# Kernel optimization log

Hardware: AMD Instinct MI355X
Metric: run time of the kernel (lower is better)

Reference implementation:

```python
import jax, jax.numpy as jnp
import numpy as np
from jax import lax

B, HI, WI, D = 8, 64, 64, 128
HO, WO = HI // 2, WI // 2
N_IN, N_OUT = HI * WI, HO * WO
NUM_ITERS = 3
EPS = 1e-6


def _build_indices(Ho, Wo):
    # replicates _build_q_and_in_idx: per coarse position, 9 relative offsets
    dys = np.repeat(np.arange(-1, 2), 3)
    dxs = np.tile(np.arange(-1, 2), 3)
    oy = np.arange(Ho)[:, None, None]
    ox = np.arange(Wo)[None, :, None]
    ny = oy + dys
    nx = ox + dxs
    valid = (ny >= 0) & (ny < Ho) & (nx >= 0) & (nx < Wo)  # (Ho,Wo,9)
    coarse = np.where(valid, ny * Wo + nx, 0)
    base = (oy * Wo + ox) * 9
    g9 = np.where(valid, base + np.arange(9), 0).reshape(-1, 9)
    c9 = coarse.reshape(-1, 9)
    q_idx = np.stack([np.tile(g9, (1, 4))] * 4)
    col_idx = np.stack([np.tile(c9, (1, 4))] * 4)
    in_idx = np.stack([np.tile(np.where(valid, coarse * 4 + h, 0).reshape(-1, 9), (1, 4)) for h in range(4)])
    return q_idx.astype(np.int32), in_idx.astype(np.int32), col_idx.astype(np.int32)


Q_IDX, IN_IDX, COL_IDX = _build_indices(HO, WO)
# NATTEN kernel-3 neighborhoods: window center clamped to stay in-bounds.
NY = np.clip(np.arange(HO) - 1, 0, HO - 3)[:, None] + np.arange(3)  # (HO,3)
NX = np.clip(np.arange(WO) - 1, 0, WO - 3)[:, None] + np.arange(3)  # (WO,3)


def _ln(x, g, b, eps=1e-5):
    mu = x.mean(-1, keepdims=True)
    var = ((x - mu) ** 2).mean(-1, keepdims=True)
    return (x - mu) * lax.rsqrt(var + eps) * g + b


def _forward(x, seed_w, wq, wk, wv, w1, b1, w2, b2, ln_in_g, ln_in_b, ln_out_g, ln_out_b, rpb, tau):
    ny, nx = jnp.asarray(NY), jnp.asarray(NX)
    q_idx = jnp.asarray(Q_IDX)

    def unfold(t):  # (B,HI,WI,D) -> (B,4,HO,WO,D); head = ky*2+kx (F.unfold order)
        return t.reshape(B, HO, 2, WO, 2, D).transpose(0, 2, 4, 1, 3, 5).reshape(B, 4, HO, WO, D)

    k = unfold((_ln(x, ln_in_g, ln_in_b) @ wk.T).reshape(B, HI, WI, D))
    v = unfold((x @ wv.T).reshape(B, HI, WI, D))
    k_n = k[:, :, ny][:, :, :, :, nx]  # (B,4,HO,3,WO,3,D)
    v_n = v[:, :, ny][:, :, :, :, nx]

    x_map = x.reshape(B, HI, WI, D).transpose(0, 3, 1, 2)
    seed = lax.conv_general_dilated(x_map, seed_w, (2, 2), ((1, 1), (1, 1)),
                                    dimension_numbers=('NCHW', 'OIHW', 'NCHW'))
    x_out = _ln(seed.reshape(B, D, N_OUT).transpose(0, 2, 1), ln_out_g, ln_out_b)

    scale = jnp.exp(tau)
    attn36 = a_col_h = None
    for _ in range(NUM_ITERS):
        q = (_ln(x_out, ln_out_g, ln_out_b) @ wq.T).reshape(B, HO, WO, D)
        # na2d_qk (q broadcast over the 4 heads) + relative position bias
        logits = jnp.einsum('byxd,bhykxld->bhyxkl', q, k_n).reshape(B, 4, HO, WO, 9) + rpb.reshape(1, 4, 1, 1, 9)
        attn = jax.nn.softmax(logits * scale, axis=-1) + EPS
        flat = attn.reshape(B, 4, N_OUT * 9)
        attn36 = jnp.take_along_axis(
            flat, jnp.broadcast_to(q_idx.reshape(1, 4, -1), (B, 4, N_OUT * 36)), axis=-1
        ).reshape(B, 4, N_OUT, 36)
        a_col_h = attn36 / (attn36.sum(axis=(1, 3), keepdims=True) + EPS)
        attn9 = a_col_h[..., :9].reshape(B, 4, HO, WO, 3, 3)
        # na2d_av then sum over heads
        updates = jnp.einsum('bhyxkl,bhykxld->byxd', attn9, v_n).reshape(B, N_OUT, D)
        x_out = x_out + updates
        h1 = jax.nn.gelu(x_out @ w1.T + b1, approximate=False)
        x_out = x_out + _ln(h1 @ w2.T + b2, ln_out_g, ln_out_b)
    return x_out, attn36, a_col_h


def setup_inputs() -> dict:
    key = jax.random.key(0)
    ks = jax.random.split(key, 8)
    n = lambda k, shape, s: jax.random.normal(k, shape, jnp.float32) * s
    D2 = 2 * D
    return {
        'x': jax.random.normal(ks[0], (B, N_IN, D), jnp.float32),
        'seed_w': n(ks[1], (D, D, 3, 3), (2.0 / (9 * D)) ** 0.5),
        'wq': n(ks[2], (D, D), D ** -0.5),
        'wk': n(ks[3], (D, D), D ** -0.5),
        'wv': n(ks[4], (D, D), D ** -0.5),
        'w1': n(ks[5], (D2, D), D ** -0.5),
        'b1': jnp.zeros((D2,), jnp.float32),
        'w2': n(ks[6], (D, D2), D2 ** -0.5),
        'b2': jnp.zeros((D,), jnp.float32),
        'ln_in_g': jnp.ones((D,), jnp.float32),
        'ln_in_b': jnp.zeros((D,), jnp.float32),
        'ln_out_g': jnp.ones((D,), jnp.float32),
        'ln_out_b': jnp.zeros((D,), jnp.float32),
        'rpb': n(ks[7], (4, 9), 0.02),
        'tau': jnp.float32(np.log(D ** -0.5)),
    }


def reference(x, seed_w, wq, wk, wv, w1, b1, w2, b2, ln_in_g, ln_in_b, ln_out_g, ln_out_b, rpb, tau):
    x_out, attn36, a_col_h = _forward(x, seed_w, wq, wk, wv, w1, b1, w2, b2,
                                      ln_in_g, ln_in_b, ln_out_g, ln_out_b, rpb, tau)
    # A_col: scatter_add over dim 1 -> A_col[b, in_idx[i,j], j] += a_col_h[b,i,j]
    rows = jnp.asarray(IN_IDX).reshape(4 * N_OUT, 36)
    cols = jnp.broadcast_to(jnp.arange(36), rows.shape)
    A_col = jnp.zeros((B, N_IN, N_OUT), x.dtype).at[:, rows, cols].add(a_col_h.reshape(B, 4 * N_OUT, 36))
    # A_row: scatter_add over dim 2 -> A_row[b, i, col_idx[i,j]] += attn36[b,i,j]
    ri = jnp.broadcast_to(jnp.arange(4 * N_OUT)[:, None], (4 * N_OUT, 36))
    A_row = jnp.zeros((B, N_IN, N_OUT), x.dtype).at[:, ri, jnp.asarray(COL_IDX).reshape(4 * N_OUT, 36)].add(
        attn36.reshape(B, 4 * N_OUT, 36))
    return x_out, A_row, A_col
```

## Files before the change

kernel.cpp:

```cpp
#include <hip/hip_runtime.h>
#include <hip/hip_bf16.h>
#include <math.h>

#define BB   8
#define HI_  64
#define WI_  64
#define DD   128
#define HO_  32
#define WO_  32
#define NIN  4096
#define NOUT 1024
#define LN_EPS 1e-5f
#define ATT_EPS 1e-6f

typedef short bf16x8 __attribute__((ext_vector_type(8)));
typedef float f32x4  __attribute__((ext_vector_type(4)));

__device__ __forceinline__ ushort f2bf(float f) {
    union { float f; unsigned u; } a; a.f = f;
    unsigned u = a.u;
    return (ushort)((u + 0x7FFFu + ((u >> 16) & 1u)) >> 16);
}
__device__ __forceinline__ float bf2f(ushort u) {
    union { unsigned u; float f; } a; a.u = ((unsigned)u) << 16;
// ... 159 lines not shown
            for (int ks = 0; ks < 2; ++ks) {
                int kk = ks * 32 + lk;
                bf16x8 aF[2];
                aF[0] = *(const bf16x8*)&As[wm + lr][kk];
                aF[1] = *(const bf16x8*)&As[wm + 16 + lr][kk];
                #pragma unroll
                for (int ni = 0; ni < 4; ++ni) {
                    bf16x8 bF = *(const bf16x8*)&Bs[wn + ni * 16 + lr][kk];
                    acc[0][ni] = __builtin_amdgcn_mfma_f32_16x16x32_bf16(aF[0], bF, acc[0][ni], 0, 0, 0);
                    acc[1][ni] = __builtin_amdgcn_mfma_f32_16x16x32_bf16(aF[1], bF, acc[1][ni], 0, 0, 0);
                }
            }
            __syncthreads();
        }
        #pragma unroll
        for (int mi = 0; mi < 2; ++mi)
            #pragma unroll
            for (int ni = 0; ni < 4; ++ni) {
                int n = wn + ni * 16 + (lane & 15);
                #pragma unroll
                for (int r = 0; r < 4; ++r)
                    es[wm + mi * 16 + ((lane >> 4) << 2) + r][n] = acc[mi][ni][r];
            }
        __syncthreads();
        {
            int r = tid >> 2, q = tid & 3;
            float s = 0.f, s2 = 0.f;
            #pragma unroll
            for (int c = 0; c < 32; ++c) { float v = es[r][q * 32 + c]; s += v; s2 += v * v; }
            s += __shfl_down(s, 1, 64); s2 += __shfl_down(s2, 1, 64);
            s += __shfl_down(s, 2, 64); s2 += __shfl_down(s2, 2, 64);
            if (q == 0) {
                float mu = s * (1.f / DD);
                float var = s2 * (1.f / DD) - mu * mu;
                rstat[r][0] = mu; rstat[r][1] = rsqrtf(var + LN_EPS);
            }
        }
        __syncthreads();
        #pragma unroll
        for (int i = 0; i < 8; ++i) {
            int l = tid + i * 256;
            int r = l >> 5, c4 = (l & 31) << 2;
            float mu = rstat[r][0], rs = rstat[r][1];
            float4 o;
            o.x = (es[r][c4 + 0] - mu) * rs * logg[c4 + 0] + lobb[c4 + 0];
            o.y = (es[r][c4 + 1] - mu) * rs * logg[c4 + 1] + lobb[c4 + 1];
            o.z = (es[r][c4 + 2] - mu) * rs * logg[c4 + 2] + lobb[c4 + 2];
            o.w = (es[r][c4 + 3] - mu) * rs * logg[c4 + 3] + lobb[c4 + 3];
            *(float4*)(xout + (size_t)(row0 + r) * DD + c4) = o;
        }
    }
}

template<int LAST>
__global__ __launch_bounds__(512, 4)
void iter_kernel(float* __restrict__ xout, const ushort* __restrict__ kbuf,
                 const ushort* __restrict__ vbuf, const ushort* __restrict__ wqb,
                 const ushort* __restrict__ w1b, const ushort* __restrict__ w2b,
                 const float* __restrict__ b1, const float* __restrict__ b2,
                 const float* __restrict__ lg_, const float* __restrict__ lb_,
                 const float* __restrict__ rpb, const float* __restrict__ tau,
                 float* __restrict__ gbuf, float* __restrict__ denb,
                 float* __restrict__ out)
{
    const int bid = blockIdx.x;
    const int b = bid >> 6, cy = (bid >> 1) & 31, cx0 = (bid & 1) << 4;
    const int ry0 = min(max(cy - 1, 0), HO_ - 3);
    const int tid = threadIdx.x;
    const int wid = tid >> 6, lane = tid & 63;
    const int lr = lane & 15, lk = (lane >> 4) << 3;

    __shared__ float  xsf[17][132];
    __shared__ ushort Aq[32][136];
    __shared__ ushort qs[17][136];
    __shared__ float  rstat[17][2];
    __shared__ float  lgp[16][36];
    __shared__ float  lg0[36];
    __shared__ float  sm0[4];
    __shared__ ushort h1s[16][264];
    __shared__ float  es[16][132];

    for (int l = tid; l < 544; l += 512) {
        int r = l >> 5, c4 = (l & 31) << 2;
        int g = b * NOUT + (r < 16 ? cy * 32 + cx0 + r : 0);
        *(float4*)&xsf[r][c4] = *(const float4*)(xout + (size_t)g * DD + c4);
    }
    __syncthreads();
    if (tid < 68) {
        int r = tid >> 2, q = tid & 3;
        float s = 0.f, s2 = 0.f;
        #pragma unroll
        for (int c = 0; c < 32; ++c) { float v = xsf[r][q * 32 + c]; s += v; s2 += v * v; }
        s += __shfl_down(s, 1, 64); s2 += __shfl_down(s2, 1, 64);
        s += __shfl_down(s, 2, 64); s2 += __shfl_down(s2, 2, 64);
        if (q == 0) {
            float mu = s * (1.f / DD);
            float var = s2 * (1.f / DD) - mu * mu;
            rstat[r][0] = mu; rstat[r][1] = rsqrtf(var + LN_EPS);
        }
    }
    __syncthreads();
    for (int l = tid; l < 544; l += 512) {
        int r = l >> 5, c4 = (l & 31) << 2;
        float mu = rstat[r][0], rs = rstat[r][1];
        ushort4 o;
        o.x = f2bf((xsf[r][c4 + 0] - mu) * rs * lg_[c4 + 0] + lb_[c4 + 0]);
        o.y = f2bf((xsf[r][c4 + 1] - mu) * rs * lg_[c4 + 1] + lb_[c4 + 1]);
        o.z = f2bf((xsf[r][c4 + 2] - mu) * rs * lg_[c4 + 2] + lb_[c4 + 2]);
        o.w = f2bf((xsf[r][c4 + 3] - mu) * rs * lg_[c4 + 3] + lb_[c4 + 3]);
        *(ushort4*)&Aq[r][c4] = o;
    }
    for (int l = tid; l < 480; l += 512) {
        int r = 17 + (l >> 5), c4 = (l & 31) << 2;
        ushort4 z; z.x = 0; z.y = 0; z.z = 0; z.w = 0;
        *(ushort4*)&Aq[r][c4] = z;
    }
    __syncthreads();

    {
        const int wn = wid * 16;
        f32x4 acc[2] = {};
        #pragma unroll
        for (int ks = 0; ks < 4; ++ks) {
            int kk = ks * 32 + lk;
            bf16x8 aF0 = *(const bf16x8*)&Aq[lr][kk];
            bf16x8 aF1 = *(const bf16x8*)&Aq[16 + lr][kk];
            bf16x8 bF = *(const bf16x8*)(wqb + (size_t)(wn + lr) * DD + kk);
            acc[0] = __builtin_amdgcn_mfma_f32_16x16x32_bf16(aF0, bF, acc[0], 0, 0, 0);
            acc[1] = __builtin_amdgcn_mfma_f32_16x16x32_bf16(aF1, bF, acc[1], 0, 0, 0);
        }
        int n = wn + (lane & 15);
        #pragma unroll
        for (int mi = 0; mi < 2; ++mi)
            #pragma unroll
            for (int r = 0; r < 4; ++r) {
                int m = mi * 16 + ((lane >> 4) << 2) + r;
                if (m < 17) qs[m][n] = f2bf(acc[mi][r]);
            }
    }
    __syncthreads();

    for (int task = tid; task < 612; task += 512) {
        const ushort *kp, *qp;
        int cl = 0, h, jj;
        if (task < 576) {
            cl = task / 36; int t2 = task - cl * 36;
            h = t2 / 9; jj = t2 - h * 9;
            int ky = jj / 3, kx = jj - ky * 3;
            int c = cx0 + cl;
            int nx = min(max(c - 1, 0), WO_ - 3) + kx;
            kp = kbuf + (((size_t)(b * 4 + h) << 10) + (ry0 + ky) * 32 + nx) * DD;
            qp = &qs[cl][0];
        } else {
            int t2 = task - 576;
            h = t2 / 9; jj = t2 - h * 9;
            int ky = jj / 3, kx = jj - ky * 3;
            kp = kbuf + (((size_t)(b * 4 + h) << 10) + ky * 32 + kx) * DD;
            qp = &qs[16][0];
        }
        float s = 0.f;
        #pragma unroll 4
        for (int d = 0; d < 128; d += 8) {
            uint4 ku = *(const uint4*)(kp + d);
            uint4 qu = *(const uint4*)(qp + d);
            const ushort* kk2 = (const ushort*)&ku;
            const ushort* qq2 = (const ushort*)&qu;
            #pragma unroll
            for (int t = 0; t < 8; ++t) s += bf2f(kk2[t]) * bf2f(qq2[t]);
        }
        if (task < 576) lgp[cl][h * 9 + jj] = s;
        else            lg0[task - 576] = s;
    }
    __syncthreads();

    if (tid < 68) {
        float scale = expf(tau[0]);
        int h; const float* lptr; int cl = 0;
        if (tid < 64) { cl = tid >> 2; h = tid & 3; lptr = &lgp[cl][h * 9]; }
        else          { h = tid - 64; lptr = &lg0[h * 9]; }
        float tmpv[9], mx = -1e30f;
        #pragma unroll
        for (int jj = 0; jj < 9; ++jj) {
            float v = (lptr[jj] + rpb[h * 9 + jj]) * scale;
            tmpv[jj] = v; mx = fmaxf(mx, v);
        }
        float ss = 0.f;
        #pragma unroll
        for (int jj = 0; jj < 9; ++jj) { tmpv[jj] = expf(tmpv[jj] - mx); ss += tmpv[jj]; }
        float inv = 1.f / ss;
        if (tid < 64) {
            #pragma unroll
            for (int jj = 0; jj < 9; ++jj) lgp[cl][h * 9 + jj] = tmpv[jj] * inv + ATT_EPS;
        } else sm0[h] = tmpv[0] * inv + ATT_EPS;
    }
    __syncthreads();

    if (tid < 64) {
        int cl = tid >> 2, h = tid & 3;
        int c = cx0 + cl;
        float s = 0.f, gv[9];
        #pragma unroll
        for (int jj = 0; jj < 9; ++jj) {
            int dy = jj / 3 - 1, dx = jj % 3 - 1;
            bool valid = ((unsigned)(cy + dy) < (unsigned)HO_) && ((unsigned)(c + dx) < (unsigned)WO_);
            float v = valid ? lgp[cl][h * 9 + jj] : sm0[h];
            gv[jj] = v; s += v;
        }
        float tot = s;
        tot += __shfl_xor(tot, 1, 4);
        tot += __shfl_xor(tot, 2, 4);
        float dd = 4.f * tot + ATT_EPS;
        if (h == 0) denb[b * NOUT + cy * 32 + cx0 + cl] = dd;
        float inv = 1.f / dd;
        float* gp = gbuf + (((size_t)(b * 4 + h) << 10) + cy * 32 + c) * 9;
        #pragma unroll
        for (int jj = 0; jj < 9; ++jj) {
            gp[jj] = gv[jj];
            lgp[cl][h * 9 + jj] = gv[jj] * inv;
        }
    }
    __syncthreads();

    {
        int cl = tid >> 5, d0 = (tid & 31) << 2;
        int c = cx0 + cl;
        int rx0 = min(max(c - 1, 0), WO_ - 3);
        float acc4[4] = {};
        #pragma unroll
        for (int h = 0; h < 4; ++h)
            #pragma unroll
            for (int jj = 0; jj < 9; ++jj) {
                float cf = lgp[cl][h * 9 + jj];
                int ky = jj / 3, kx = jj - ky * 3;
                const ushort* vp = vbuf + (((size_t)(b * 4 + h) << 10) + (ry0 + ky) * 32 + rx0 + kx) * DD + d0;
                uint2 v0 = *(const uint2*)(vp);
                const ushort* vs0 = (const ushort*)&v0;
                #pragma unroll
                for (int t = 0; t < 4; ++t) acc4[t] += cf * bf2f(vs0[t]);
            }
        float4 o = *(float4*)&xsf[cl][d0];
        o.x += acc4[0]; o.y += acc4[1]; o.z += acc4[2]; o.w += acc4[3];
        *(float4*)&xsf[cl][d0] = o;
    }
    __syncthreads();

    {
        int l = tid;
        int r = l >> 5, c4 = (l & 31) << 2;
        ushort4 o;
        o.x = f2bf(xsf[r][c4 + 0]); o.y = f2bf(xsf[r][c4 + 1]);
        o.z = f2bf(xsf[r][c4 + 2]); o.w = f2bf(xsf[r][c4 + 3]);
        *(ushort4*)&Aq[r][c4] = o;
    }
    __syncthreads();
    {
        const int wn = wid * 32;
        f32x4 acc[2] = {};
        #pragma unroll
        for (int ks = 0; ks < 4; ++ks) {
            int kk = ks * 32 + lk;
            bf16x8 a0 = *(const bf16x8*)&Aq[lr][kk];
            #pragma unroll
            for (int ni = 0; ni < 2; ++ni) {
                bf16x8 bF = *(const bf16x8*)(w1b + (size_t)(wn + ni * 16 + lr) * DD + kk);
                acc[ni] = __builtin_amdgcn_mfma_f32_16x16x32_bf16(a0, bF, acc[ni], 0, 0, 0);
            }
        }
        #pragma unroll
        for (int ni = 0; ni < 2; ++ni) {
            int n = wn + ni * 16 + (lane & 15);
            float bv = b1[n];
            #pragma unroll
            for (int r = 0; r < 4; ++r) {
                int m = ((lane >> 4) << 2) + r;
                float v = acc[ni][r] + bv;
                v = 0.5f * v * (1.f + erff(v * 0.70710678118654752f));
                h1s[m][n] = f2bf(v);
            }
        }
    }
    __syncthreads();

    {
        const int wn = wid * 16;
        f32x4 acc = {};
        #pragma unroll
        for (int ks = 0; ks < 8; ++ks) {
            int kk = ks * 32 + lk;
            bf16x8 a0 = *(const bf16x8*)&h1s[lr][kk];
            bf16x8 bF = *(const bf16x8*)(w2b + (size_t)(wn + lr) * 256 + kk);
            acc = __builtin_amdgcn_mfma_f32_16x16x32_bf16(a0, bF, acc, 0, 0, 0);
        }
        int n = wn + (lane & 15);
        float bv = b2[n];
        #pragma unroll
        for (int r = 0; r < 4; ++r)
            es[((lane >> 4) << 2) + r][n] = acc[r] + bv;
    }
    __syncthreads();
    if (tid < 128) {
        int r = tid >> 3, qq = tid & 7;
        float s = 0.f, s2 = 0.f;
        #pragma unroll
        for (int c = 0; c < 16; ++c) { float v = es[r][qq * 16 + c]; s += v; s2 += v * v; }
        s += __shfl_down(s, 1, 64); s2 += __shfl_down(s2, 1, 64);
        s += __shfl_down(s, 2, 64); s2 += __shfl_down(s2, 2, 64);
        s += __shfl_down(s, 4, 64); s2 += __shfl_down(s2, 4, 64);
        if (qq == 0) {
            float mu = s * (1.f / DD);
            float var = s2 * (1.f / DD) - mu * mu;
            rstat[r][0] = mu; rstat[r][1] = rsqrtf(var + LN_EPS);
        }
    }
    __syncthreads();
    {
        int l = tid;
        int r = l >> 5, c4 = (l & 31) << 2;
        float mu = rstat[r][0], rs = rstat[r][1];
        size_t off = ((size_t)(b * NOUT + cy * 32 + cx0 + r)) * DD + c4;
        float4 o;
        o.x = xsf[r][c4 + 0] + (es[r][c4 + 0] - mu) * rs * lg_[c4 + 0] + lb_[c4 + 0];
        o.y = xsf[r][c4 + 1] + (es[r][c4 + 1] - mu) * rs * lg_[c4 + 1] + lb_[c4 + 1];
        o.z = xsf[r][c4 + 2] + (es[r][c4 + 2] - mu) * rs * lg_[c4 + 2] + lb_[c4 + 2];
        o.w = xsf[r][c4 + 3] + (es[r][c4 + 3] - mu) * rs * lg_[c4 + 3] + lb_[c4 + 3];
        *(float4*)(xout + off) = o;
        if (LAST) *(float4*)(out + off) = o;
    }
}

__global__ __launch_bounds__(256)
void arowcol_kernel(const float* __restrict__ gbuf, const float* __restrict__ denb,
                    float* __restrict__ Arow, float* __restrict__ Acol)
{
    const int tid = threadIdx.x;
    __shared__ int   cols[9];
    __shared__ float vals[9];
    __shared__ float wred[9][4];
    if (blockIdx.x < 32768) {
        const int bi = blockIdx.x;
        const int b = bi >> 12, i = bi & 4095;
        const int h = i >> 10, p = i & 1023;
        const int cy = p >> 5, cx = p & 31;
        if (tid < 9) {
            int dy = tid / 3 - 1, dx = tid % 3 - 1;
            bool valid = ((unsigned)(cy + dy) < (unsigned)HO_) && ((unsigned)(cx + dx) < (unsigned)WO_);
            cols[tid] = valid ? (cy + dy) * WO_ + (cx + dx) : 0;
            vals[tid] = 4.f * gbuf[(((size_t)(b * 4 + h) << 10) + p) * 9 + tid];
        }
        __syncthreads();
        float* row = Arow + (size_t)bi * NOUT;
        #pragma unroll
        for (int cc = 0; cc < 4; ++cc) {
            int c = cc * 256 + tid;
            float acc = 0.f;
            #pragma unroll
            for (int jj = 0; jj < 9; ++jj)
                if (cols[jj] == c) acc += vals[jj];
            row[c] = acc;
        }
    } else {
        const int br = blockIdx.x - 32768;
        const int b = br >> 12, r = br & 4095;
        const int h = r & 3, coarse = r >> 2;
        const int cy = coarse >> 5, cx = coarse & 31;
        if (tid < 9) {
            int dy = tid / 3 - 1, dx = tid % 3 - 1;
            int py = cy - dy, px = cx - dx;
            float v = 0.f;
            if ((unsigned)py < (unsigned)HO_ && (unsigned)px < (unsigned)WO_) {
                int p = py * WO_ + px;
                v = gbuf[(((size_t)(b * 4 + h) << 10) + p) * 9 + tid] / denb[b * NOUT + p];
            }
            vals[tid] = v;
        }
        if (r == 0) {
            float part[9] = {};
            for (int p = tid; p < NOUT; p += 256) {
                float invd = 1.f / denb[b * NOUT + p];
                int py = p >> 5, px = p & 31;
                #pragma unroll
                for (int jj = 0; jj < 9; ++jj) {
                    int dy = jj / 3 - 1, dx = jj % 3 - 1;
                    bool valid = ((unsigned)(py + dy) < (unsigned)HO_) && ((unsigned)(px + dx) < (unsigned)WO_);
                    if (!valid) part[jj] += invd;
                }
            }
            #pragma unroll
            for (int jj = 0; jj < 9; ++jj) {
                float s = part[jj];
                #pragma unroll
                for (int o = 32; o > 0; o >>= 1) s += __shfl_down(s, o, 64);
                if ((tid & 63) == 0) wred[jj][tid >> 6] = s;
            }
            __syncthreads();
            if (tid < 9) {
                float s = wred[tid][0] + wred[tid][1] + wred[tid][2] + wred[tid][3];
                float H = 0.f;
                for (int h2 = 0; h2 < 4; ++h2)
                    H += gbuf[(((size_t)(b * 4 + h2)) << 10) * 9];
                vals[tid] += H * s;
            }
        }
        __syncthreads();
        float* row = Acol + (size_t)br * NOUT;
        #pragma unroll
        for (int cc = 0; cc < 4; ++cc) {
            int c = cc * 256 + tid;
            row[c] = (c < 36) ? vals[c % 9] : 0.f;
        }
    }
}

extern "C" void kernel_launch(void* const* d_in, const int* in_sizes, int n_in,
                              void* d_out, int out_size, void* d_ws, size_t ws_size,
                              hipStream_t stream)
{
    const float* x        = (const float*)d_in[0];
    const float* seed_w   = (const float*)d_in[1];
    const float* wq       = (const float*)d_in[2];
    const float* wk       = (const float*)d_in[3];
    const float* wv       = (const float*)d_in[4];
    const float* w1       = (const float*)d_in[5];
    const float* b1       = (const float*)d_in[6];
    const float* w2       = (const float*)d_in[7];
    const float* b2       = (const float*)d_in[8];
    const float* ln_in_g  = (const float*)d_in[9];
    const float* ln_in_b  = (const float*)d_in[10];
    const float* ln_out_g = (const float*)d_in[11];
    const float* ln_out_b = (const float*)d_in[12];
    const float* rpb      = (const float*)d_in[13];
    const float* tau      = (const float*)d_in[14];

    float* out  = (float*)d_out;
    float* Arow = out + (size_t)BB * NOUT * DD;
    float* Acol = Arow + (size_t)BB * NIN * NOUT;

    float* ws    = (float*)d_ws;
    float* xout  = ws;
    float* gbuf  = xout + (size_t)BB * NOUT * DD;
    float* denb  = gbuf + (size_t)BB * 4 * NOUT * 9;
    ushort* wb   = (ushort*)(denb + BB * NOUT);
    ushort* wkb  = wb;
    ushort* wvb  = wb + 16384;
    ushort* wqb  = wb + 32768;
    ushort* w1b  = wb + 49152;
    ushort* w2b  = wb + 81920;
    ushort* wcb  = wb + 114688;

    ushort* kbuf = (ushort*)Arow;
    ushort* vbuf = kbuf + (size_t)4194304;

    wconvert_kernel<<<1024, 256, 0, stream>>>(wq, wk, wv, w1, w2, seed_w, wb);
    prep_kernel<<<640, 256, 0, stream>>>(x, wkb, wvb, wcb, ln_in_g, ln_in_b,
                                         ln_out_g, ln_out_b, kbuf, vbuf, xout);

    for (int it = 0; it < 3; ++it) {
        if (it < 2)
            iter_kernel<0><<<BB * HO_ * 2, 512, 0, stream>>>(
                xout, kbuf, vbuf, wqb, w1b, w2b, b1, b2, ln_out_g, ln_out_b,
                rpb, tau, gbuf, denb, out);
        else
            iter_kernel<1><<<BB * HO_ * 2, 512, 0, stream>>>(
                xout, kbuf, vbuf, wqb, w1b, w2b, b1, b2, ln_out_g, ln_out_b,
                rpb, tau, gbuf, denb, out);
    }

    arowcol_kernel<<<2 * BB * NIN, 256, 0, stream>>>(gbuf, denb, Arow, Acol);
}
```

Baseline: 193.6 us.

## Fuse three iteration launches into one persistent kernel with redundant query-0 row

Folds the three slot-attention iteration launches into a single kernel that keeps each block's 16 query rows in shared memory across iterations. Because every block now recomputes the coarse position 0 query (row 16) locally instead of reading it from a global buffer updated by the previous launch, the cross-block dependency disappears and the full pipeline (LN, MLP, attention) is extended to 17 rows. Block size drops from 512 to 256 threads, and the Arow/Acol writer switches to float4 stores. This removes two launches and the global round-trips of xout, at the cost of extra redundant work for the shared row and fewer threads per block.

Result: slower. 230.8 us (+19.2%).

```diff
diff --git a/kernel.cpp b/kernel.cpp
--- a/kernel.cpp
+++ b/kernel.cpp
@@ -235,16 +235,15 @@
     }
 }
 
-template<int LAST>
-__global__ __launch_bounds__(512, 4)
-void iter_kernel(float* __restrict__ xout, const ushort* __restrict__ kbuf,
-                 const ushort* __restrict__ vbuf, const ushort* __restrict__ wqb,
-                 const ushort* __restrict__ w1b, const ushort* __restrict__ w2b,
-                 const float* __restrict__ b1, const float* __restrict__ b2,
-                 const float* __restrict__ lg_, const float* __restrict__ lb_,
-                 const float* __restrict__ rpb, const float* __restrict__ tau,
-                 float* __restrict__ gbuf, float* __restrict__ denb,
-                 float* __restrict__ out)
+__global__ __launch_bounds__(256)
+void iter_all_kernel(const float* __restrict__ xout, const ushort* __restrict__ kbuf,
+                     const ushort* __restrict__ vbuf, const ushort* __restrict__ wqb,
+                     const ushort* __restrict__ w1b, const ushort* __restrict__ w2b,
+                     const float* __restrict__ b1, const float* __restrict__ b2,
+                     const float* __restrict__ lg_, const float* __restrict__ lb_,
+                     const float* __restrict__ rpb, const float* __restrict__ tau,
+                     float* __restrict__ gbuf, float* __restrict__ denb,
+                     float* __restrict__ out)
 {
     const int bid = blockIdx.x;
     const int b = bid >> 6, cy = (bid >> 1) & 31, cx0 = (bid & 1) << 4;
@@ -257,257 +256,289 @@
     __shared__ ushort Aq[32][136];
     __shared__ ushort qs[17][136];
     __shared__ float  rstat[17][2];
-    __shared__ float  lgp[16][36];
+    __shared__ float  lgp[17][36];
     __shared__ float  lg0[36];
     __shared__ float  sm0[4];
-    __shared__ ushort h1s[16][264];
-    __shared__ float  es[16][132];
-
-    for (int l = tid; l < 544; l += 512) {
+    __shared__ ushort h1s[17][264];
+    __shared__ float  es[17][132];
+
+    for (int l = tid; l < 544; l += 256) {
         int r = l >> 5, c4 = (l & 31) << 2;
         int g = b * NOUT + (r < 16 ? cy * 32 + cx0 + r : 0);
         *(float4*)&xsf[r][c4] = *(const float4*)(xout + (size_t)g * DD + c4);
     }
-    __syncthreads();
-    if (tid < 68) {
-        int r = tid >> 2, q = tid & 3;
-        float s = 0.f, s2 = 0.f;
-        #pragma unroll
-        for (int c = 0; c < 32; ++c) { float v = xsf[r][q * 32 + c]; s += v; s2 += v * v; }
-        s += __shfl_down(s, 1, 64); s2 += __shfl_down(s2, 1, 64);
-        s += __shfl_down(s, 2, 64); s2 += __shfl_down(s2, 2, 64);
-        if (q == 0) {
-            float mu = s * (1.f / DD);
-            float var = s2 * (1.f / DD) - mu * mu;
-            rstat[r][0] = mu; rstat[r][1] = rsqrtf(var + LN_EPS);
-        }
-    }
-    __syncthreads();
-    for (int l = tid; l < 544; l += 512) {
-        int r = l >> 5, c4 = (l & 31) << 2;
-        float mu = rstat[r][0], rs = rstat[r][1];
-        ushort4 o;
-        o.x = f2bf((xsf[r][c4 + 0] - mu) * rs * lg_[c4 + 0] + lb_[c4 + 0]);
-        o.y = f2bf((xsf[r][c4 + 1] - mu) * rs * lg_[c4 + 1] + lb_[c4 + 1]);
-        o.z = f2bf((xsf[r][c4 + 2] - mu) * rs * lg_[c4 + 2] + lb_[c4 + 2]);
-        o.w = f2bf((xsf[r][c4 + 3] - mu) * rs * lg_[c4 + 3] + lb_[c4 + 3]);
-        *(ushort4*)&Aq[r][c4] = o;
-    }
-    for (int l = tid; l < 480; l += 512) {
-        int r = 17 + (l >> 5), c4 = (l & 31) << 2;
-        ushort4 z; z.x = 0; z.y = 0; z.z = 0; z.w = 0;
-        *(ushort4*)&Aq[r][c4] = z;
-    }
-    __syncthreads();
-
-    {
-        const int wn = wid * 16;
-        f32x4 acc[2] = {};
-        #pragma unroll
-        for (int ks = 0; ks < 4; ++ks) {
-            int kk = ks * 32 + lk;
-            bf16x8 aF0 = *(const bf16x8*)&Aq[lr][kk];
-            bf16x8 aF1 = *(const bf16x8*)&Aq[16 + lr][kk];
-            bf16x8 bF = *(const bf16x8*)(wqb + (size_t)(wn + lr) * DD + kk);
-            acc[0] = __builtin_amdgcn_mfma_f32_16x16x32_bf16(aF0, bF, acc[0], 0, 0, 0);
-            acc[1] = __builtin_amdgcn_mfma_f32_16x16x32_bf16(aF1, bF, acc[1], 0, 0, 0);
-        }
-        int n = wn + (lane & 15);
-        #pragma unroll
-        for (int mi = 0; mi < 2; ++mi)
-            #pragma unroll
-            for (int r = 0; r < 4; ++r) {
-                int m = mi * 16 + ((lane >> 4) << 2) + r;
-                if (m < 17) qs[m][n] = f2bf(acc[mi][r]);
-            }
-    }
-    __syncthreads();
-
-    for (int task = tid; task < 612; task += 512) {
-        const ushort *kp, *qp;
-        int cl = 0, h, jj;
-        if (task < 576) {
-            cl = task / 36; int t2 = task - cl * 36;
-            h = t2 / 9; jj = t2 - h * 9;
-            int ky = jj / 3, kx = jj - ky * 3;
-            int c = cx0 + cl;
-            int nx = min(max(c - 1, 0), WO_ - 3) + kx;
-            kp = kbuf + (((size_t)(b * 4 + h) << 10) + (ry0 + ky) * 32 + nx) * DD;
-            qp = &qs[cl][0];
-        } else {
-            int t2 = task - 576;
-            h = t2 / 9; jj = t2 - h * 9;
-            int ky = jj / 3, kx = jj - ky * 3;
-            kp = kbuf + (((size_t)(b * 4 + h) << 10) + ky * 32 + kx) * DD;
-            qp = &qs[16][0];
-        }
-        float s = 0.f;
-        #pragma unroll 4
-        for (int d = 0; d < 128; d += 8) {
-            uint4 ku = *(const uint4*)(kp + d);
-            uint4 qu = *(const uint4*)(qp + d);
-            const ushort* kk2 = (const ushort*)&ku;
-            const ushort* qq2 = (const ushort*)&qu;
-            #pragma unroll
-            for (int t = 0; t < 8; ++t) s += bf2f(kk2[t]) * bf2f(qq2[t]);
-        }
-        if (task < 576) lgp[cl][h * 9 + jj] = s;
-        else            lg0[task - 576] = s;
-    }
-    __syncthreads();
-
-    if (tid < 68) {
-        float scale = expf(tau[0]);
-        int h; const float* lptr; int cl = 0;
-        if (tid < 64) { cl = tid >> 2; h = tid & 3; lptr = &lgp[cl][h * 9]; }
-        else          { h = tid - 64; lptr = &lg0[h * 9]; }
-        float tmpv[9], mx = -1e30f;
-        #pragma unroll
-        for (int jj = 0; jj < 9; ++jj) {
-            float v = (lptr[jj] + rpb[h * 9 + jj]) * scale;
-            tmpv[jj] = v; mx = fmaxf(mx, v);
-        }
-        float ss = 0.f;
-        #pragma unroll
-        for (int jj = 0; jj < 9; ++jj) { tmpv[jj] = expf(tmpv[jj] - mx); ss += tmpv[jj]; }
-        float inv = 1.f / ss;
-        if (tid < 64) {
-            #pragma unroll
-            for (int jj = 0; jj < 9; ++jj) lgp[cl][h * 9 + jj] = tmpv[jj] * inv + ATT_EPS;
-        } else sm0[h] = tmpv[0] * inv + ATT_EPS;
-    }
-    __syncthreads();
-
-    if (tid < 64) {
-        int cl = tid >> 2, h = tid & 3;
-        int c = cx0 + cl;
-        float s = 0.f, gv[9];
-        #pragma unroll
-        for (int jj = 0; jj < 9; ++jj) {
-            int dy = jj / 3 - 1, dx = jj % 3 - 1;
-            bool valid = ((unsigned)(cy + dy) < (unsigned)HO_) && ((unsigned)(c + dx) < (unsigned)WO_);
-            float v = valid ? lgp[cl][h * 9 + jj] : sm0[h];
-            gv[jj] = v; s += v;
-        }
-        float tot = s;
-        tot += __shfl_xor(tot, 1, 4);
-        tot += __shfl_xor(tot, 2, 4);
-        float dd = 4.f * tot + ATT_EPS;
-        if (h == 0) denb[b * NOUT + cy * 32 + cx0 + cl] = dd;
-        float inv = 1.f / dd;
-        float* gp = gbuf + (((size_t)(b * 4 + h) << 10) + cy * 32 + c) * 9;
-        #pragma unroll
-        for (int jj = 0; jj < 9; ++jj) {
-            gp[jj] = gv[jj];
-            lgp[cl][h * 9 + jj] = gv[jj] * inv;
-        }
-    }
-    __syncthreads();
-
-    {
-        int cl = tid >> 5, d0 = (tid & 31) << 2;
-        int c = cx0 + cl;
-        int rx0 = min(max(c - 1, 0), WO_ - 3);
-        float acc4[4] = {};
-        #pragma unroll
-        for (int h = 0; h < 4; ++h)
+
+    for (int it = 0; it < 3; ++it) {
+        __syncthreads();
+        if (tid < 68) {
+            int r = tid >> 2, q = tid & 3;
+            float s = 0.f, s2 = 0.f;
+            #pragma unroll
+            for (int c = 0; c < 32; ++c) { float v = xsf[r][q * 32 + c]; s += v; s2 += v * v; }
+            s += __shfl_down(s, 1, 64); s2 += __shfl_down(s2, 1, 64);
+            s += __shfl_down(s, 2, 64); s2 += __shfl_down(s2, 2, 64);
+            if (q == 0) {
+                float mu = s * (1.f / DD);
+                float var = s2 * (1.f / DD) - mu * mu;
+                rstat[r][0] = mu; rstat[r][1] = rsqrtf(var + LN_EPS);
+            }
+        }
+        __syncthreads();
+        for (int l = tid; l < 544; l += 256) {
+            int r = l >> 5, c4 = (l & 31) << 2;
+            float mu = rstat[r][0], rs = rstat[r][1];
+            ushort4 o;
+            o.x = f2bf((xsf[r][c4 + 0] - mu) * rs * lg_[c4 + 0] + lb_[c4 + 0]);
+            o.y = f2bf((xsf[r][c4 + 1] - mu) * rs * lg_[c4 + 1] + lb_[c4 + 1]);
+            o.z = f2bf((xsf[r][c4 + 2] - mu) * rs * lg_[c4 + 2] + lb_[c4 + 2]);
+            o.w = f2bf((xsf[r][c4 + 3] - mu) * rs * lg_[c4 + 3] + lb_[c4 + 3]);
+            *(ushort4*)&Aq[r][c4] = o;
+        }
+        __syncthreads();
+
+        {
+            const int wn = wid * 32;
+            f32x4 acc[2][2] = {};
+            #pragma unroll
+            for (int ks = 0; ks < 4; ++ks) {
+                int kk = ks * 32 + lk;
+                bf16x8 aF0 = *(const bf16x8*)&Aq[lr][kk];
+                bf16x8 aF1 = *(const bf16x8*)&Aq[16 + lr][kk];
+                #pragma unroll
+                for (int ni = 0; ni < 2; ++ni) {
+                    bf16x8 bF = *(const bf16x8*)(wqb + (size_t)(wn + ni * 16 + lr) * DD + kk);
+                    acc[0][ni] = __builtin_amdgcn_mfma_f32_16x16x32_bf16(aF0, bF, acc[0][ni], 0, 0, 0);
+                    acc[1][ni] = __builtin_amdgcn_mfma_f32_16x16x32_bf16(aF1, bF, acc[1][ni], 0, 0, 0);
+                }
+            }
+            #pragma unroll
+            for (int mi = 0; mi < 2; ++mi)
+                #pragma unroll
+                for (int ni = 0; ni < 2; ++ni) {
+                    int n = wn + ni * 16 + (lane & 15);
+                    #pragma unroll
+                    for (int r = 0; r < 4; ++r) {
+                        int m = mi * 16 + ((lane >> 4) << 2) + r;
+                        if (m < 17) qs[m][n] = f2bf(acc[mi][ni][r]);
+                    }
+                }
+        }
+        __syncthreads();
+
+        for (int task = tid; task < 612; task += 256) {
+            const ushort *kp, *qp;
+            int cl = 0, h, jj;
+            if (task < 576) {
+                cl = task / 36; int t2 = task - cl * 36;
+                h = t2 / 9; jj = t2 - h * 9;
+                int ky = jj / 3, kx = jj - ky * 3;
+                int c = cx0 + cl;
+                int nx = min(max(c - 1, 0), WO_ - 3) + kx;
+                kp = kbuf + (((size_t)(b * 4 + h) << 10) + (ry0 + ky) * 32 + nx) * DD;
+                qp = &qs[cl][0];
+            } else {
+                int t2 = task - 576;
+                h = t2 / 9; jj = t2 - h * 9;
+                int ky = jj / 3, kx = jj - ky * 3;
+                kp = kbuf + (((size_t)(b * 4 + h) << 10) + ky * 32 + kx) * DD;
+                qp = &qs[16][0];
+            }
+            float s = 0.f;
+            #pragma unroll 4
+            for (int d = 0; d < 128; d += 8) {
+                uint4 ku = *(const uint4*)(kp + d);
+                uint4 qu = *(const uint4*)(qp + d);
+                const ushort* kk2 = (const ushort*)&ku;
+                const ushort* qq2 = (const ushort*)&qu;
+                #pragma unroll
+                for (int t = 0; t < 8; ++t) s += bf2f(kk2[t]) * bf2f(qq2[t]);
+            }
+            if (task < 576) lgp[cl][h * 9 + jj] = s;
+            else            lg0[task - 576] = s;
+        }
+        __syncthreads();
+
+        if (tid < 68) {
+            float scale = expf(tau[0]);
+            int h; const float* lptr; int cl = 0;
+            if (tid < 64) { cl = tid >> 2; h = tid & 3; lptr = &lgp[cl][h * 9]; }
+            else          { h = tid - 64; lptr = &lg0[h * 9]; }
+            float tmpv[9], mx = -1e30f;
             #pragma unroll
             for (int jj = 0; jj < 9; ++jj) {
-                float cf = lgp[cl][h * 9 + jj];
-                int ky = jj / 3, kx = jj - ky * 3;
-                const ushort* vp = vbuf + (((size_t)(b * 4 + h) << 10) + (ry0 + ky) * 32 + rx0 + kx) * DD + d0;
-                uint2 v0 = *(const uint2*)(vp);
-                const ushort* vs0 = (const ushort*)&v0;
-                #pragma unroll
-                for (int t = 0; t < 4; ++t) acc4[t] += cf * bf2f(vs0[t]);
-            }
-        float4 o = *(float4*)&xsf[cl][d0];
-        o.x += acc4[0]; o.y += acc4[1]; o.z += acc4[2]; o.w += acc4[3];
-        *(float4*)&xsf[cl][d0] = o;
-    }
-    __syncthreads();
-
-    {
-        int l = tid;
-        int r = l >> 5, c4 = (l & 31) << 2;
-        ushort4 o;
-        o.x = f2bf(xsf[r][c4 + 0]); o.y = f2bf(xsf[r][c4 + 1]);
-        o.z = f2bf(xsf[r][c4 + 2]); o.w = f2bf(xsf[r][c4 + 3]);
-        *(ushort4*)&Aq[r][c4] = o;
-    }
-    __syncthreads();
-    {
-        const int wn = wid * 32;
-        f32x4 acc[2] = {};
-        #pragma unroll
-        for (int ks = 0; ks < 4; ++ks) {
-            int kk = ks * 32 + lk;
-            bf16x8 a0 = *(const bf16x8*)&Aq[lr][kk];
-            #pragma unroll
-            for (int ni = 0; ni < 2; ++ni) {
-                bf16x8 bF = *(const bf16x8*)(w1b + (size_t)(wn + ni * 16 + lr) * DD + kk);
-                acc[ni] = __builtin_amdgcn_mfma_f32_16x16x32_bf16(a0, bF, acc[ni], 0, 0, 0);
-            }
-        }
-        #pragma unroll
-        for (int ni = 0; ni < 2; ++ni) {
-            int n = wn + ni * 16 + (lane & 15);
-            float bv = b1[n];
-            #pragma unroll
-            for (int r = 0; r < 4; ++r) {
-                int m = ((lane >> 4) << 2) + r;
-                float v = acc[ni][r] + bv;
-                v = 0.5f * v * (1.f + erff(v * 0.70710678118654752f));
-                h1s[m][n] = f2bf(v);
-            }
-        }
-    }
-    __syncthreads();
-
-    {
-        const int wn = wid * 16;
-        f32x4 acc = {};
-        #pragma unroll
-        for (int ks = 0; ks < 8; ++ks) {
-            int kk = ks * 32 + lk;
-            bf16x8 a0 = *(const bf16x8*)&h1s[lr][kk];
-            bf16x8 bF = *(const bf16x8*)(w2b + (size_t)(wn + lr) * 256 + kk);
-            acc = __builtin_amdgcn_mfma_f32_16x16x32_bf16(a0, bF, acc, 0, 0, 0);
-        }
-        int n = wn + (lane & 15);
-        float bv = b2[n];
-        #pragma unroll
-        for (int r = 0; r < 4; ++r)
-            es[((lane >> 4) << 2) + r][n] = acc[r] + bv;
-    }
-    __syncthreads();
-    if (tid < 128) {
-        int r = tid >> 3, qq = tid & 7;
-        float s = 0.f, s2 = 0.f;
-        #pragma unroll
-        for (int c = 0; c < 16; ++c) { float v = es[r][qq * 16 + c]; s += v; s2 += v * v; }
-        s += __shfl_down(s, 1, 64); s2 += __shfl_down(s2, 1, 64);
-        s += __shfl_down(s, 2, 64); s2 += __shfl_down(s2, 2, 64);
-        s += __shfl_down(s, 4, 64); s2 += __shfl_down(s2, 4, 64);
-        if (qq == 0) {
-            float mu = s * (1.f / DD);
-            float var = s2 * (1.f / DD) - mu * mu;
-            rstat[r][0] = mu; rstat[r][1] = rsqrtf(var + LN_EPS);
-        }
-    }
-    __syncthreads();
-    {
-        int l = tid;
-        int r = l >> 5, c4 = (l & 31) << 2;
-        float mu = rstat[r][0], rs = rstat[r][1];
-        size_t off = ((size_t)(b * NOUT + cy * 32 + cx0 + r)) * DD + c4;
-        float4 o;
-        o.x = xsf[r][c4 + 0] + (es[r][c4 + 0] - mu) * rs * lg_[c4 + 0] + lb_[c4 + 0];
-        o.y = xsf[r][c4 + 1] + (es[r][c4 + 1] - mu) * rs * lg_[c4 + 1] + lb_[c4 + 1];
-        o.z = xsf[r][c4 + 2] + (es[r][c4 + 2] - mu) * rs * lg_[c4 + 2] + lb_[c4 + 2];
-        o.w = xsf[r][c4 + 3] + (es[r][c4 + 3] - mu) * rs * lg_[c4 + 3] + lb_[c4 + 3];
-        *(float4*)(xout + off) = o;
-        if (LAST) *(float4*)(out + off) = o;
+                float v = (lptr[jj] + rpb[h * 9 + jj]) * scale;
+                tmpv[jj] = v; mx = fmaxf(mx, v);
+            }
+            float ss = 0.f;
+            #pragma unroll
+            for (int jj = 0; jj < 9; ++jj) { tmpv[jj] = expf(tmpv[jj] - mx); ss += tmpv[jj]; }
+            float inv = 1.f / ss;
+            if (tid < 64) {
+                #pragma unroll
+                for (int jj = 0; jj < 9; ++jj) lgp[cl][h * 9 + jj] = tmpv[jj] * inv + ATT_EPS;
+            } else {
+                #pragma unroll
+                for (int jj = 0; jj < 9; ++jj) lgp[16][h * 9 + jj] = tmpv[jj] * inv + ATT_EPS;
+                sm0[h] = tmpv[0] * inv + ATT_EPS;
+            }
+        }
+        __syncthreads();
+
+        if (tid < 68) {
+            int cl = tid >> 2, h = tid & 3;
+            int ecy = (cl < 16) ? cy : 0;
+            int ec  = (cl < 16) ? (cx0 + cl) : 0;
+            float s = 0.f, gv[9];
+            #pragma unroll
+            for (int jj = 0; jj < 9; ++jj) {
+                int dy = jj / 3 - 1, dx = jj % 3 - 1;
+                bool valid = ((unsigned)(ecy + dy) < (unsigned)HO_) && ((unsigned)(ec + dx) < (unsigned)WO_);
+                float v = valid ? lgp[cl][h * 9 + jj] : sm0[h];
+                gv[jj] = v; s += v;
+            }
+            float tot = s;
+            tot += __shfl_xor(tot, 1, 4);
+            tot += __shfl_xor(tot, 2, 4);
+            float dd = 4.f * tot + ATT_EPS;
+            float inv = 1.f / dd;
+            if (it == 2 && cl < 16) {
+                if (h == 0) denb[b * NOUT + cy * 32 + cx0 + cl] = dd;
+                float* gp = gbuf + (((size_t)(b * 4 + h) << 10) + cy * 32 + ec) * 9;
+                #pragma unroll
+                for (int jj = 0; jj < 9; ++jj) gp[jj] = gv[jj];
+            }
+            #pragma unroll
+            for (int jj = 0; jj < 9; ++jj) lgp[cl][h * 9 + jj] = gv[jj] * inv;
+        }
+        __syncthreads();
+
+        for (int t = tid; t < 272; t += 256) {
+            int cl = t >> 4, d0 = (t & 15) << 3;
+            int ery0 = (cl < 16) ? ry0 : 0;
+            int erx0 = (cl < 16) ? min(max(cx0 + cl - 1, 0), WO_ - 3) : 0;
+            float acc8[8] = {};
+            #pragma unroll
+            for (int h = 0; h < 4; ++h)
+                #pragma unroll
+                for (int jj = 0; jj < 9; ++jj) {
+                    float cf = lgp[cl][h * 9 + jj];
+                    int ky = jj / 3, kx = jj - ky * 3;
+                    const ushort* vp = vbuf + (((size_t)(b * 4 + h) << 10) + (ery0 + ky) * 32 + erx0 + kx) * DD + d0;
+                    uint4 v0 = *(const uint4*)(vp);
+                    const ushort* vs0 = (const ushort*)&v0;
+                    #pragma unroll
+                    for (int e = 0; e < 8; ++e) acc8[e] += cf * bf2f(vs0[e]);
+                }
+            #pragma unroll
+            for (int e = 0; e < 8; e += 4) {
+                float4 o = *(float4*)&xsf[cl][d0 + e];
+                o.x += acc8[e]; o.y += acc8[e + 1]; o.z += acc8[e + 2]; o.w += acc8[e + 3];
+                *(float4*)&xsf[cl][d0 + e] = o;
+            }
+        }
+        __syncthreads();
+
+        for (int l = tid; l < 544; l += 256) {
+            int r = l >> 5, c4 = (l & 31) << 2;
+            ushort4 o;
+            o.x = f2bf(xsf[r][c4 + 0]); o.y = f2bf(xsf[r][c4 + 1]);
+            o.z = f2bf(xsf[r][c4 + 2]); o.w = f2bf(xsf[r][c4 + 3]);
+            *(ushort4*)&Aq[r][c4] = o;
+        }
+        __syncthreads();
+
+        {
+            const int wn = wid * 64;
+            f32x4 acc[2][4] = {};
+            #pragma unroll
+            for (int ks = 0; ks < 4; ++ks) {
+                int kk = ks * 32 + lk;
+                bf16x8 a0 = *(const bf16x8*)&Aq[lr][kk];
+                bf16x8 a1 = *(const bf16x8*)&Aq[16 + lr][kk];
+                #pragma unroll
+                for (int ni = 0; ni < 4; ++ni) {
+                    bf16x8 bF = *(const bf16x8*)(w1b + (size_t)(wn + ni * 16 + lr) * DD + kk);
+                    acc[0][ni] = __builtin_amdgcn_mfma_f32_16x16x32_bf16(a0, bF, acc[0][ni], 0, 0, 0);
+                    acc[1][ni] = __builtin_amdgcn_mfma_f32_16x16x32_bf16(a1, bF, acc[1][ni], 0, 0, 0);
+                }
+            }
+            #pragma unroll
+            for (int mi = 0; mi < 2; ++mi)
+                #pragma unroll
+                for (int ni = 0; ni < 4; ++ni) {
+                    int n = wn + ni * 16 + (lane & 15);
+                    float bv = b1[n];
+                    #pragma unroll
+                    for (int r = 0; r < 4; ++r) {
+                        int m = mi * 16 + ((lane >> 4) << 2) + r;
+                        if (m < 17) {
+                            float v = acc[mi][ni][r] + bv;
+                            v = 0.5f * v * (1.f + erff(v * 0.70710678118654752f));
+                            h1s[m][n] = f2bf(v);
+                        }
+                    }
+                }
+        }
+        __syncthreads();
+
+        {
+            const int wn = wid * 32;
+            f32x4 acc[2][2] = {};
+            #pragma unroll
+            for (int ks = 0; ks < 8; ++ks) {
+                int kk = ks * 32 + lk;
+                bf16x8 a0 = *(const bf16x8*)&h1s[lr][kk];
+                bf16x8 a1 = *(const bf16x8*)&h1s[16 + lr][kk];
+                #pragma unroll
+                for (int ni = 0; ni < 2; ++ni) {
+                    bf16x8 bF = *(const bf16x8*)(w2b + (size_t)(wn + ni * 16 + lr) * 256 + kk);
+                    acc[0][ni] = __builtin_amdgcn_mfma_f32_16x16x32_bf16(a0, bF, acc[0][ni], 0, 0, 0);
+                    acc[1][ni] = __builtin_amdgcn_mfma_f32_16x16x32_bf16(a1, bF, acc[1][ni], 0, 0, 0);
+                }
+            }
+            #pragma unroll
+            for (int mi = 0; mi < 2; ++mi)
+                #pragma unroll
+                for (int ni = 0; ni < 2; ++ni) {
+                    int n = wn + ni * 16 + (lane & 15);
+                    float bv = b2[n];
+                    #pragma unroll
+                    for (int r = 0; r < 4; ++r) {
+                        int m = mi * 16 + ((lane >> 4) << 2) + r;
+                        if (m < 17) es[m][n] = acc[mi][ni][r] + bv;
+                    }
+                }
+        }
+        __syncthreads();
+
+        if (tid < 136) {
+            int r = tid >> 3, qq = tid & 7;
+            float s = 0.f, s2 = 0.f;
+            #pragma unroll
+            for (int c = 0; c < 16; ++c) { float v = es[r][qq * 16 + c]; s += v; s2 += v * v; }
+            s += __shfl_down(s, 1, 64); s2 += __shfl_down(s2, 1, 64);
+            s += __shfl_down(s, 2, 64); s2 += __shfl_down(s2, 2, 64);
+            s += __shfl_down(s, 4, 64); s2 += __shfl_down(s2, 4, 64);
+            if (qq == 0) {
+                float mu = s * (1.f / DD);
+                float var = s2 * (1.f / DD) - mu * mu;
+                rstat[r][0] = mu; rstat[r][1] = rsqrtf(var + LN_EPS);
+            }
+        }
+        __syncthreads();
+
+        for (int l = tid; l < 544; l += 256) {
+            int r = l >> 5, c4 = (l & 31) << 2;
+            float mu = rstat[r][0], rs = rstat[r][1];
+            float4 o;
+            o.x = xsf[r][c4 + 0] + (es[r][c4 + 0] - mu) * rs * lg_[c4 + 0] + lb_[c4 + 0];
+            o.y = xsf[r][c4 + 1] + (es[r][c4 + 1] - mu) * rs * lg_[c4 + 1] + lb_[c4 + 1];
+            o.z = xsf[r][c4 + 2] + (es[r][c4 + 2] - mu) * rs * lg_[c4 + 2] + lb_[c4 + 2];
+            o.w = xsf[r][c4 + 3] + (es[r][c4 + 3] - mu) * rs * lg_[c4 + 3] + lb_[c4 + 3];
+            *(float4*)&xsf[r][c4] = o;
+            if (it == 2 && r < 16)
+                *(float4*)(out + ((size_t)(b * NOUT + cy * 32 + cx0 + r)) * DD + c4) = o;
+        }
     }
 }
 
@@ -532,15 +563,14 @@
         }
         __syncthreads();
         float* row = Arow + (size_t)bi * NOUT;
-        #pragma unroll
-        for (int cc = 0; cc < 4; ++cc) {
-            int c = cc * 256 + tid;
-            float acc = 0.f;
+        int c4 = tid << 2;
+        float o[4] = {};
+        #pragma unroll
+        for (int e = 0; e < 4; ++e)
             #pragma unroll
             for (int jj = 0; jj < 9; ++jj)
-                if (cols[jj] == c) acc += vals[jj];
-            row[c] = acc;
-        }
+                if (cols[jj] == c4 + e) o[e] += vals[jj];
+        *(float4*)(row + c4) = make_float4(o[0], o[1], o[2], o[3]);
     } else {
         const int br = blockIdx.x - 32768;
         const int b = br >> 12, r = br & 4095;
@@ -586,11 +616,14 @@
         }
         __syncthreads();
         float* row = Acol + (size_t)br * NOUT;
-        #pragma unroll
-        for (int cc = 0; cc < 4; ++cc) {
-            int c = cc * 256 + tid;
-            row[c] = (c < 36) ? vals[c % 9] : 0.f;
-        }
+        int c4 = tid << 2;
+        float o[4];
+        #pragma unroll
+        for (int e = 0; e < 4; ++e) {
+            int c = c4 + e;
+            o[e] = (c < 36) ? vals[c % 9] : 0.f;
+        }
+        *(float4*)(row + c4) = make_float4(o[0], o[1], o[2], o[3]);
     }
 }
 
@@ -637,16 +670,9 @@
     prep_kernel<<<640, 256, 0, stream>>>(x, wkb, wvb, wcb, ln_in_g, ln_in_b,
                                          ln_out_g, ln_out_b, kbuf, vbuf, xout);
 
-    for (int it = 0; it < 3; ++it) {
-        if (it < 2)
-            iter_kernel<0><<<BB * HO_ * 2, 512, 0, stream>>>(
-                xout, kbuf, vbuf, wqb, w1b, w2b, b1, b2, ln_out_g, ln_out_b,
-                rpb, tau, gbuf, denb, out);
-        else
-            iter_kernel<1><<<BB * HO_ * 2, 512, 0, stream>>>(
-                xout, kbuf, vbuf, wqb, w1b, w2b, b1, b2, ln_out_g, ln_out_b,
-                rpb, tau, gbuf, denb, out);
-    }
+    iter_all_kernel<<<BB * HO_ * 2, 256, 0, stream>>>(
+        xout, kbuf, vbuf, wqb, w1b, w2b, b1, b2, ln_out_g, ln_out_b,
+        rpb, tau, gbuf, denb, out);
 
     arowcol_kernel<<<2 * BB * NIN, 256, 0, stream>>>(gbuf, denb, Arow, Acol);
 }
```

## Halve iter_kernel block size and vectorize A_row/A_col stores as float4

Applied to the files above, without the earlier changes.

Reduces iter_kernel from 512 to 256 threads per block. Each wave now computes more MFMA output tiles in the Q, W1 and W2 GEMMs, and the value aggregation loads 8 bf16 per thread instead of 4. Zeroing of the unused Aq padding rows is dropped, because those rows only feed discarded output rows. Separately, arowcol_kernel writes each output row with one float4 store per thread instead of four scalar stores, which cuts the store instruction count on the large A_row/A_col fill. The cost is more work and registers per thread in iter_kernel and fewer threads to hide memory latency.

Result: no change. 192.7 us (-0.5%).

```diff
diff --git a/kernel.cpp b/kernel.cpp
--- a/kernel.cpp
+++ b/kernel.cpp
@@ -236,7 +236,7 @@
 }
 
 template<int LAST>
-__global__ __launch_bounds__(512, 4)
+__global__ __launch_bounds__(256)
 void iter_kernel(float* __restrict__ xout, const ushort* __restrict__ kbuf,
                  const ushort* __restrict__ vbuf, const ushort* __restrict__ wqb,
                  const ushort* __restrict__ w1b, const ushort* __restrict__ w2b,
@@ -263,7 +263,7 @@
     __shared__ ushort h1s[16][264];
     __shared__ float  es[16][132];
 
-    for (int l = tid; l < 544; l += 512) {
+    for (int l = tid; l < 544; l += 256) {
         int r = l >> 5, c4 = (l & 31) << 2;
         int g = b * NOUT + (r < 16 ? cy * 32 + cx0 + r : 0);
         *(float4*)&xsf[r][c4] = *(const float4*)(xout + (size_t)g * DD + c4);
@@ -283,7 +283,7 @@
         }
     }
     __syncthreads();
-    for (int l = tid; l < 544; l += 512) {
+    for (int l = tid; l < 544; l += 256) {
         int r = l >> 5, c4 = (l & 31) << 2;
         float mu = rstat[r][0], rs = rstat[r][1];
         ushort4 o;
@@ -293,37 +293,38 @@
         o.w = f2bf((xsf[r][c4 + 3] - mu) * rs * lg_[c4 + 3] + lb_[c4 + 3]);
         *(ushort4*)&Aq[r][c4] = o;
     }
-    for (int l = tid; l < 480; l += 512) {
-        int r = 17 + (l >> 5), c4 = (l & 31) << 2;
-        ushort4 z; z.x = 0; z.y = 0; z.z = 0; z.w = 0;
-        *(ushort4*)&Aq[r][c4] = z;
-    }
     __syncthreads();
 
     {
-        const int wn = wid * 16;
-        f32x4 acc[2] = {};
+        const int wn = wid * 32;
+        f32x4 acc[2][2] = {};
         #pragma unroll
         for (int ks = 0; ks < 4; ++ks) {
             int kk = ks * 32 + lk;
             bf16x8 aF0 = *(const bf16x8*)&Aq[lr][kk];
             bf16x8 aF1 = *(const bf16x8*)&Aq[16 + lr][kk];
-            bf16x8 bF = *(const bf16x8*)(wqb + (size_t)(wn + lr) * DD + kk);
-            acc[0] = __builtin_amdgcn_mfma_f32_16x16x32_bf16(aF0, bF, acc[0], 0, 0, 0);
-            acc[1] = __builtin_amdgcn_mfma_f32_16x16x32_bf16(aF1, bF, acc[1], 0, 0, 0);
-        }
-        int n = wn + (lane & 15);
+            #pragma unroll
+            for (int ni = 0; ni < 2; ++ni) {
+                bf16x8 bF = *(const bf16x8*)(wqb + (size_t)(wn + ni * 16 + lr) * DD + kk);
+                acc[0][ni] = __builtin_amdgcn_mfma_f32_16x16x32_bf16(aF0, bF, acc[0][ni], 0, 0, 0);
+                acc[1][ni] = __builtin_amdgcn_mfma_f32_16x16x32_bf16(aF1, bF, acc[1][ni], 0, 0, 0);
+            }
+        }
         #pragma unroll
         for (int mi = 0; mi < 2; ++mi)
             #pragma unroll
-            for (int r = 0; r < 4; ++r) {
-                int m = mi * 16 + ((lane >> 4) << 2) + r;
-                if (m < 17) qs[m][n] = f2bf(acc[mi][r]);
-            }
-    }
-    __syncthreads();
-
-    for (int task = tid; task < 612; task += 512) {
+            for (int ni = 0; ni < 2; ++ni) {
+                int n = wn + ni * 16 + (lane & 15);
+                #pragma unroll
+                for (int r = 0; r < 4; ++r) {
+                    int m = mi * 16 + ((lane >> 4) << 2) + r;
+                    if (m < 17) qs[m][n] = f2bf(acc[mi][ni][r]);
+                }
+            }
+    }
+    __syncthreads();
+
+    for (int task = tid; task < 612; task += 256) {
         const ushort *kp, *qp;
         int cl = 0, h, jj;
         if (task < 576) {
@@ -405,10 +406,10 @@
     __syncthreads();
 
     {
-        int cl = tid >> 5, d0 = (tid & 31) << 2;
+        int cl = tid >> 4, d0 = (tid & 15) << 3;
         int c = cx0 + cl;
         int rx0 = min(max(c - 1, 0), WO_ - 3);
-        float acc4[4] = {};
+        float acc8[8] = {};
         #pragma unroll
         for (int h = 0; h < 4; ++h)
             #pragma unroll
@@ -416,19 +417,21 @@
                 float cf = lgp[cl][h * 9 + jj];
                 int ky = jj / 3, kx = jj - ky * 3;
                 const ushort* vp = vbuf + (((size_t)(b * 4 + h) << 10) + (ry0 + ky) * 32 + rx0 + kx) * DD + d0;
-                uint2 v0 = *(const uint2*)(vp);
+                uint4 v0 = *(const uint4*)(vp);
                 const ushort* vs0 = (const ushort*)&v0;
                 #pragma unroll
-                for (int t = 0; t < 4; ++t) acc4[t] += cf * bf2f(vs0[t]);
-            }
-        float4 o = *(float4*)&xsf[cl][d0];
-        o.x += acc4[0]; o.y += acc4[1]; o.z += acc4[2]; o.w += acc4[3];
-        *(float4*)&xsf[cl][d0] = o;
-    }
-    __syncthreads();
-
-    {
-        int l = tid;
+                for (int t = 0; t < 8; ++t) acc8[t] += cf * bf2f(vs0[t]);
+            }
+        #pragma unroll
+        for (int t = 0; t < 8; t += 4) {
+            float4 o = *(float4*)&xsf[cl][d0 + t];
+            o.x += acc8[t]; o.y += acc8[t + 1]; o.z += acc8[t + 2]; o.w += acc8[t + 3];
+            *(float4*)&xsf[cl][d0 + t] = o;
+        }
+    }
+    __syncthreads();
+
+    for (int l = tid; l < 512; l += 256) {
         int r = l >> 5, c4 = (l & 31) << 2;
         ushort4 o;
         o.x = f2bf(xsf[r][c4 + 0]); o.y = f2bf(xsf[r][c4 + 1]);
@@ -437,20 +440,20 @@
     }
     __syncthreads();
     {
-        const int wn = wid * 32;
-        f32x4 acc[2] = {};
+        const int wn = wid * 64;
+        f32x4 acc[4] = {};
         #pragma unroll
         for (int ks = 0; ks < 4; ++ks) {
             int kk = ks * 32 + lk;
             bf16x8 a0 = *(const bf16x8*)&Aq[lr][kk];
             #pragma unroll
-            for (int ni = 0; ni < 2; ++ni) {
+            for (int ni = 0; ni < 4; ++ni) {
                 bf16x8 bF = *(const bf16x8*)(w1b + (size_t)(wn + ni * 16 + lr) * DD + kk);
                 acc[ni] = __builtin_amdgcn_mfma_f32_16x16x32_bf16(a0, bF, acc[ni], 0, 0, 0);
             }
         }
         #pragma unroll
-        for (int ni = 0; ni < 2; ++ni) {
+        for (int ni = 0; ni < 4; ++ni) {
             int n = wn + ni * 16 + (lane & 15);
             float bv = b1[n];
             #pragma unroll
@@ -465,20 +468,26 @@
     __syncthreads();
 
     {
-        const int wn = wid * 16;
-        f32x4 acc = {};
+        const int wn = wid * 32;
+        f32x4 acc[2] = {};
         #pragma unroll
         for (int ks = 0; ks < 8; ++ks) {
             int kk = ks * 32 + lk;
             bf16x8 a0 = *(const bf16x8*)&h1s[lr][kk];
-            bf16x8 bF = *(const bf16x8*)(w2b + (size_t)(wn + lr) * 256 + kk);
-            acc = __builtin_amdgcn_mfma_f32_16x16x32_bf16(a0, bF, acc, 0, 0, 0);
-        }
-        int n = wn + (lane & 15);
-        float bv = b2[n];
-        #pragma unroll
-        for (int r = 0; r < 4; ++r)
-            es[((lane >> 4) << 2) + r][n] = acc[r] + bv;
+            #pragma unroll
+            for (int ni = 0; ni < 2; ++ni) {
+                bf16x8 bF = *(const bf16x8*)(w2b + (size_t)(wn + ni * 16 + lr) * 256 + kk);
+                acc[ni] = __builtin_amdgcn_mfma_f32_16x16x32_bf16(a0, bF, acc[ni], 0, 0, 0);
+            }
+        }
+        #pragma unroll
+        for (int ni = 0; ni < 2; ++ni) {
+            int n = wn + ni * 16 + (lane & 15);
+            float bv = b2[n];
+            #pragma unroll
+            for (int r = 0; r < 4; ++r)
+                es[((lane >> 4) << 2) + r][n] = acc[ni][r] + bv;
+        }
     }
     __syncthreads();
     if (tid < 128) {
@@ -496,8 +505,7 @@
         }
     }
     __syncthreads();
-    {
-        int l = tid;
+    for (int l = tid; l < 512; l += 256) {
         int r = l >> 5, c4 = (l & 31) << 2;
         float mu = rstat[r][0], rs = rstat[r][1];
         size_t off = ((size_t)(b * NOUT + cy * 32 + cx0 + r)) * DD + c4;
@@ -532,15 +540,14 @@
         }
         __syncthreads();
         float* row = Arow + (size_t)bi * NOUT;
-        #pragma unroll
-        for (int cc = 0; cc < 4; ++cc) {
-            int c = cc * 256 + tid;
-            float acc = 0.f;
+        int c4 = tid << 2;
+        float o[4] = {};
+        #pragma unroll
+        for (int e = 0; e < 4; ++e)
             #pragma unroll
             for (int jj = 0; jj < 9; ++jj)
-                if (cols[jj] == c) acc += vals[jj];
-            row[c] = acc;
-        }
+                if (cols[jj] == c4 + e) o[e] += vals[jj];
+        *(float4*)(row + c4) = make_float4(o[0], o[1], o[2], o[3]);
     } else {
         const int br = blockIdx.x - 32768;
         const int b = br >> 12, r = br & 4095;
@@ -586,11 +593,14 @@
         }
         __syncthreads();
         float* row = Acol + (size_t)br * NOUT;
-        #pragma unroll
-        for (int cc = 0; cc < 4; ++cc) {
-            int c = cc * 256 + tid;
-            row[c] = (c < 36) ? vals[c % 9] : 0.f;
-        }
+        int c4 = tid << 2;
+        float o[4];
+        #pragma unroll
+        for (int e = 0; e < 4; ++e) {
+            int c = c4 + e;
+            o[e] = (c < 36) ? vals[c % 9] : 0.f;
+        }
+        *(float4*)(row + c4) = make_float4(o[0], o[1], o[2], o[3]);
     }
 }
 
@@ -639,11 +649,11 @@
 
     for (int it = 0; it < 3; ++it) {
         if (it < 2)
-            iter_kernel<0><<<BB * HO_ * 2, 512, 0, stream>>>(
+            iter_kernel<0><<<BB * HO_ * 2, 256, 0, stream>>>(
                 xout, kbuf, vbuf, wqb, w1b, w2b, b1, b2, ln_out_g, ln_out_b,
                 rpb, tau, gbuf, denb, out);
         else
-            iter_kernel<1><<<BB * HO_ * 2, 512, 0, stream>>>(
+            iter_kernel<1><<<BB * HO_ * 2, 256, 0, stream>>>(
                 xout, kbuf, vbuf, wqb, w1b, w2b, b1, b2, ln_out_g, ln_out_b,
                 rpb, tau, gbuf, denb, out);
     }
```
